# Optimization experiments

Hardware: AMD Instinct MI355X
Metric: run time of the kernel (lower is better)

The kernel has to match this reference:

```python
import jax, jax.numpy as jnp
import numpy as np

N_NODES = 20000
N_RELS = 64
RP = 8
EMB = 64
N_CLASSES = 16
NT = 250000      # unique (subject, object) pairs
N_TRIPLES = 500000


def setup_inputs() -> dict:
    rng = np.random.default_rng(0)
    # sample candidate (s, o) pairs, dedupe (mirrors torch.unique(pairs, dim=0)),
    # keep exactly NT unique pairs
    cand = rng.integers(0, N_NODES, size=(NT + 60000, 2))
    pairs = np.unique(cand, axis=0)
    assert pairs.shape[0] >= NT
    pairs = pairs[:NT]
    # each triple maps to a unique-pair row and a relation column;
    # relation_matrix is the coalesced sparse_coo (nt, num_rels) densified
    row = rng.integers(0, NT, size=N_TRIPLES)
    rel = rng.integers(0, N_RELS, size=N_TRIPLES)
    relation_matrix = np.zeros((NT, N_RELS), dtype=np.float32)
    np.add.at(relation_matrix, (row, rel), 1.0)
    # hindices / vindices exactly as in __init__ (note the literal o*r / s*r):
    s, o = pairs[:, 0].astype(np.int64), pairs[:, 1].astype(np.int64)
    rm = np.arange(RP, dtype=np.int64)[:, None]
    hrow = np.tile(s, RP)                      # (RP*NT,) row in [0, N)
    hcol = (o[None, :] * rm).reshape(-1)       # (RP*NT,) col in [0, N*RP)
    vrow = (s[None, :] * rm).reshape(-1)       # (RP*NT,) row in [0, N*RP)
    vcol = np.tile(o, RP)                      # (RP*NT,) col in [0, N)

    key = jax.random.key(0)
    ks = jax.random.split(key, 6)

    def xavier(k, shape, fan_in, fan_out):
        gain = np.float32(np.sqrt(2.0))  # calculate_gain('relu')
        bound = gain * np.float32(np.sqrt(6.0 / (fan_in + fan_out)))
        return jax.random.uniform(k, shape, jnp.float32, -bound, bound)

    lb = np.float32(1.0 / np.sqrt(N_RELS))  # nn.Linear default init bound
    return {
        "relation_matrix": jnp.asarray(relation_matrix),
        "hrow": jnp.asarray(hrow), "hcol": jnp.asarray(hcol),
        "vrow": jnp.asarray(vrow), "vcol": jnp.asarray(vcol),
        "W_l1": jax.random.uniform(ks[0], (N_RELS, RP), jnp.float32, -lb, lb),
        "b_l1": jax.random.uniform(ks[1], (RP,), jnp.float32, -lb, lb),
        "W_l2": jax.random.uniform(ks[2], (N_RELS, RP), jnp.float32, -lb, lb),
        "b_l2": jax.random.uniform(ks[3], (RP,), jnp.float32, -lb, lb),
        "weights1": xavier(ks[4], (RP, N_NODES, EMB), N_NODES * EMB, RP * EMB),
        "weights2": xavier(ks[5], (RP, EMB, N_CLASSES), EMB * N_CLASSES, RP * N_CLASSES),
        "bias1": jnp.zeros((EMB,), jnp.float32),
        "bias2": jnp.zeros((N_CLASSES,), jnp.float32),
    }


def reference(relation_matrix, hrow, hcol, vrow, vcol,
              W_l1, b_l1, W_l2, b_l2, weights1, weights2, bias1, bias2):
    n, rp, e = N_NODES, RP, EMB
    nrp = n * rp
    # ---- hop 1: latent coefficients (to_latent1, ldepth=0 => single Linear)
    l1 = relation_matrix @ W_l1 + b_l1              # (NT, RP)
    l1 = l1.T.reshape(-1)                           # (RP*NT,) r-major, matches h/v index order
    # sum_sparse(hindices, l1, (n, n*rp), row=False): per-edge column-sum normalization
    colsum = jax.ops.segment_sum(l1, hcol, num_segments=nrp)
    l1 = l1 / colsum[hcol]
    # spmm over hindices: out[hrow] += l1 * weights1.view(n*rp, e)[hcol]
    Wflat = weights1.reshape(nrp, e)                # (N*RP, EMB)
    h = jax.ops.segment_sum(l1[:, None] * Wflat[hcol], hrow, num_segments=n)
    h = jax.nn.relu(h + bias1)                      # (N, EMB)
    # ---- hop 2
    l2 = jax.nn.softmax(relation_matrix @ W_l2 + b_l2, axis=1)  # (NT, RP)
    l2 = jax.nn.relu(l2.T.reshape(-1))              # (RP*NT,)
    # sum_sparse(vindices, l2, (n*rp, n), row=True): per-edge row-sum normalization
    rowsum = jax.ops.segment_sum(l2, vrow, num_segments=nrp)
    l2 = l2 / jnp.maximum(rowsum[vrow], 1e-6)
    # spmm over vindices: out[vrow] += l2 * h[vcol]
    h2 = jax.ops.segment_sum(l2[:, None] * h[vcol], vrow, num_segments=nrp)
    h2 = h2.reshape(rp, n, e)                       # (RP, N, EMB)
    logits = jnp.einsum('rhc,rnh->nc', weights2, h2) + bias2  # (N, C)
    return logits
```

## Files before the change

### kernel.cpp

```cpp
#include <hip/hip_runtime.h>
#include <hip/hip_fp16.h>

#define NT      250000
#define NN      20000
#define RP      8
#define EMB     64
#define NCLS    16
#define NRELS   64
#define REDB    64
#define KMAX    140000
#define GEMVB   977
#define RPB     79
#define HIB     977
#define MISCB   1250

__global__ __launch_bounds__(256) void k_gemv(
    const float* __restrict__ rm,
    const float* __restrict__ W1, const float* __restrict__ b1,
    const float* __restrict__ W2, const float* __restrict__ b2,
    float* __restrict__ l1, float* __restrict__ l2,
    const int* __restrict__ hrow, int* __restrict__ rowptr,
    const int* __restrict__ vcol, int* __restrict__ cnt)
{
    __shared__ float tile[256 * 20];
    int bid = blockIdx.x;
    if (bid >= GEMVB) {
        int b = bid - GEMVB;
        if (b < RPB) {
            int i = b * 256 + threadIdx.x;
            if (i > NN) return;
            int lo = 0, hi = NT;
            while (lo < hi) { int mid = (lo + hi) >> 1; if (hrow[mid] < i) lo = mid + 1; else hi = mid; }
            rowptr[i] = lo;
        } else {
            int p = (b - RPB) * 256 + threadIdx.x;
            if (p < NT) atomicAdd(&cnt[vcol[p]], 1);
        }
        return;
    }
    int t = threadIdx.x;
    int base = bid * 256;
    float a1[8], a2[8];
#pragma unroll
    for (int r = 0; r < 8; ++r) { a1[r] = b1[r]; a2[r] = b2[r]; }

#pragma unroll 1
    for (int kc = 0; kc < 4; ++kc) {
        __syncthreads();
#pragma unroll
        for (int q = 0; q < 4; ++q) {
            int i = q * 256 + t;
            int pl = i >> 2, j4 = i & 3;
            int p = base + pl;
            float4 v = make_float4(0.f, 0.f, 0.f, 0.f);
            if (p < NT) v = reinterpret_cast<const float4*>(rm)[(size_t)p * 16 + kc * 4 + j4];
            *reinterpret_cast<float4*>(&tile[pl * 20 + j4 * 4]) = v;
        }
        __syncthreads();
        float xr[16];
#pragma unroll
        for (int j4 = 0; j4 < 4; ++j4) {
            float4 v = *reinterpret_cast<const float4*>(&tile[t * 20 + j4 * 4]);
            xr[j4 * 4 + 0] = v.x; xr[j4 * 4 + 1] = v.y;
            xr[j4 * 4 + 2] = v.z; xr[j4 * 4 + 3] = v.w;
        }
#pragma unroll
        for (int kk = 0; kk < 16; ++kk) {
            float x = xr[kk];
            int k = kc * 16 + kk;
#pragma unroll
            for (int r = 0; r < 8; ++r) {
                a1[r] = fmaf(x, W1[k * 8 + r], a1[r]);
                a2[r] = fmaf(x, W2[k * 8 + r], a2[r]);
            }
        }
    }
    int p = base + t;
    if (p >= NT) return;
    float mx = a2[0];
#pragma unroll
    for (int r = 1; r < 8; ++r) mx = fmaxf(mx, a2[r]);
    float sm = 0.f;
#pragma unroll
    for (int r = 0; r < 8; ++r) { a2[r] = __expf(a2[r] - mx); sm += a2[r]; }
    float inv = 1.0f / sm;
#pragma unroll
    for (int r = 0; r < 8; ++r) a2[r] *= inv;
    float4* o1 = reinterpret_cast<float4*>(l1 + (size_t)p * 8);
    float4* o2 = reinterpret_cast<float4*>(l2 + (size_t)p * 8);
    o1[0] = make_float4(a1[0], a1[1], a1[2], a1[3]);
    o1[1] = make_float4(a1[4], a1[5], a1[6], a1[7]);
    o2[0] = make_float4(a2[0], a2[1], a2[2], a2[3]);
    o2[1] = make_float4(a2[4], a2[5], a2[6], a2[7]);
}

__global__ __launch_bounds__(1024) void k_scan(
    const int* __restrict__ cnt, int* __restrict__ cstart, int* __restrict__ cnt2)
{
    __shared__ int part[1024];
    int t = threadIdx.x;
    int base = t * 20;
    int local[20];
    int s = 0;
#pragma unroll
    for (int i = 0; i < 20; ++i) {
        int idx = base + i;
        int c = (idx < NN) ? cnt[idx] : 0;
        local[i] = s;
        s += c;
    }
    part[t] = s;
    __syncthreads();
    for (int off = 1; off < 1024; off <<= 1) {
        int v = (t >= off) ? part[t - off] : 0;
        __syncthreads();
        part[t] += v;
        __syncthreads();
    }
    int ebase = t ? part[t - 1] : 0;
#pragma unroll
    for (int i = 0; i < 20; ++i) {
        int idx = base + i;
        if (idx < NN) { cstart[idx] = ebase + local[i]; cnt2[idx] = ebase + local[i]; }
    }
    if (t == 1023) cstart[NN] = part[1023];
}

__global__ __launch_bounds__(256) void k_pos(
    const int* __restrict__ vcol, int* __restrict__ cnt2, int* __restrict__ cscidx)
{
    int p = blockIdx.x * blockDim.x + threadIdx.x;
    if (p >= NT) return;
    int o = vcol[p];
    int slot = atomicAdd(&cnt2[o], 1);
    cscidx[slot] = p;
}

__global__ __launch_bounds__(256) void k_colsum(
    const float* __restrict__ l1, const int* __restrict__ cstart,
    const int* __restrict__ cscidx, float* __restrict__ colsum)
{
    int bid = blockIdx.x;
    if (bid < NN / 4) {
        int o = bid * 4 + (threadIdx.x >> 6);
        int lane = threadIdx.x & 63;
        int qb = cstart[o], qe = cstart[o + 1];
        if (qb == qe) return;
        int j = lane >> 3, r = lane & 7;
        float sum = 0.f;
        for (int q0 = qb; q0 < qe; q0 += 8) {
            int q = q0 + j;
            if (q < qe) sum += l1[(size_t)cscidx[q] * 8 + r];
        }
        sum += __shfl_xor(sum, 8, 64);
        sum += __shfl_xor(sum, 16, 64);
        sum += __shfl_xor(sum, 32, 64);
        if (lane >= 1 && lane < 8) atomicAdd(&colsum[o * lane], sum);
    } else {
        int b2 = bid - NN / 4;
        float s = 0.f;
        for (int i = b2 * 256 + threadIdx.x; i < NT; i += REDB * 256) s += l1[(size_t)i * 8];
        __shared__ float red[256];
        red[threadIdx.x] = s;
        __syncthreads();
        for (int off = 128; off > 0; off >>= 1) {
            if (threadIdx.x < off) red[threadIdx.x] += red[threadIdx.x + off];
            __syncthreads();
        }
        if (threadIdx.x == 0) atomicAdd(&colsum[0], red[0]);
    }
}

__global__ __launch_bounds__(256) void k_contrib(
    const float* __restrict__ l1, const float* __restrict__ colsum,
    const int* __restrict__ cstart, const int* __restrict__ cscidx,
    const float* __restrict__ w1, __half* __restrict__ contrib)
{
    int o = (int)((blockIdx.x * blockDim.x + threadIdx.x) >> 6);
    int lane = threadIdx.x & 63;
    if (o >= NN) return;
    int qb = cstart[o], qe = cstart[o + 1];
    if (qb == qe) return;
    float y[8];
    y[0] = w1[lane] / colsum[0];
#pragma unroll
    for (int r = 1; r < 8; ++r) {
        int seg = o * r;
        y[r] = w1[(size_t)seg * EMB + lane] / colsum[seg];
    }
    int q = qb;
    for (; q + 1 < qe; q += 2) {
        int p0 = cscidx[q], p1 = cscidx[q + 1];
        const float4* a4 = reinterpret_cast<const float4*>(l1 + (size_t)p0 * 8);
        const float4* b4 = reinterpret_cast<const float4*>(l1 + (size_t)p1 * 8);
        float4 A = a4[0], B = a4[1], C = b4[0], D = b4[1];
        float v0 = A.x * y[0];
        v0 = fmaf(A.y, y[1], v0); v0 = fmaf(A.z, y[2], v0); v0 = fmaf(A.w, y[3], v0);
        v0 = fmaf(B.x, y[4], v0); v0 = fmaf(B.y, y[5], v0);
        v0 = fmaf(B.z, y[6], v0); v0 = fmaf(B.w, y[7], v0);
        float v1 = C.x * y[0];
        v1 = fmaf(C.y, y[1], v1); v1 = fmaf(C.z, y[2], v1); v1 = fmaf(C.w, y[3], v1);
        v1 = fmaf(D.x, y[4], v1); v1 = fmaf(D.y, y[5], v1);
        v1 = fmaf(D.z, y[6], v1); v1 = fmaf(D.w, y[7], v1);
        contrib[(size_t)p0 * EMB + lane] = __float2half(v0);
        contrib[(size_t)p1 * EMB + lane] = __float2half(v1);
    }
    if (q < qe) {
        int p0 = cscidx[q];
        const float4* a4 = reinterpret_cast<const float4*>(l1 + (size_t)p0 * 8);
        float4 A = a4[0], B = a4[1];
        float v0 = A.x * y[0];
        v0 = fmaf(A.y, y[1], v0); v0 = fmaf(A.z, y[2], v0); v0 = fmaf(A.w, y[3], v0);
        v0 = fmaf(B.x, y[4], v0); v0 = fmaf(B.y, y[5], v0);
        v0 = fmaf(B.z, y[6], v0); v0 = fmaf(B.w, y[7], v0);
        contrib[(size_t)p0 * EMB + lane] = __float2half(v0);
    }
}

__global__ __launch_bounds__(256) void k_h(
    const __half* __restrict__ contrib, const float* __restrict__ l2,
    const int* __restrict__ rowptr, const float* __restrict__ bias1,
    __half* __restrict__ h, float* __restrict__ rowsum, float* __restrict__ rs0part)
{
    int s = (int)((blockIdx.x * blockDim.x + threadIdx.x) >> 6);
    int lane = threadIdx.x & 63;
    if (s >= NN) return;
    int pb = rowptr[s], pe = rowptr[s + 1];
    float acc = 0.f;
    for (int p = pb; p < pe; ++p)
        acc += __half2float(contrib[(size_t)p * EMB + lane]);
    h[(size_t)s * EMB + lane] = __float2half(fmaxf(acc + bias1[lane], 0.f));

    float psum = 0.f;
    for (int p0 = pb + (lane >> 3); p0 < pe; p0 += 8)
        psum += l2[(size_t)p0 * 8 + (lane & 7)];
    psum += __shfl_xor(psum, 8, 64);
    psum += __shfl_xor(psum, 16, 64);
    psum += __shfl_xor(psum, 32, 64);
    if (s == 0) {
        float tt = psum;
        tt += __shfl_xor(tt, 1, 64);
        tt += __shfl_xor(tt, 2, 64);
        tt += __shfl_xor(tt, 4, 64);
        if (lane == 0) rs0part[0] = tt;
    } else {
        if (lane == 0) rs0part[s] = psum;
        else if (lane < 8) atomicAdd(&rowsum[s * lane], psum);
    }
}

__global__ __launch_bounds__(256) void k_misc(
    float* __restrict__ rs, float* __restrict__ out, const float* __restrict__ b2,
    const float* __restrict__ rs0part)
{
    int bid = blockIdx.x;
    if (bid < MISCB) {
        int i = bid * 256 + threadIdx.x;
        if (i >= 1 && i < KMAX) rs[i] = 1.0f / fmaxf(rs[i], 1e-6f);
        if (i < NN * NCLS) out[i] = b2[i & (NCLS - 1)];
    } else {
        __shared__ float red[256];
        float sv = 0.f;
        for (int i = threadIdx.x; i < NN; i += 256) sv += rs0part[i];
        red[threadIdx.x] = sv;
        __syncthreads();
        for (int off = 128; off > 0; off >>= 1) {
            if (threadIdx.x < off) red[threadIdx.x] += red[threadIdx.x + off];
            __syncthreads();
        }
        if (threadIdx.x == 0) rs[0] = 1.0f / fmaxf(red[0], 1e-6f);
    }
}

__global__ __launch_bounds__(256) void k_l2out(
    const float* __restrict__ l2, const int* __restrict__ rowptr,
    const int* __restrict__ vcol, const __half* __restrict__ h,
    const float* __restrict__ irs, const float* __restrict__ w2,
    float* __restrict__ out, float* __restrict__ Abuf0)
{
    int s = (int)((blockIdx.x * blockDim.x + threadIdx.x) >> 6);
    int lane = threadIdx.x & 63;
    if (s >= NN) return;
    int pb = rowptr[s], pe = rowptr[s + 1];
    float sc[8];
#pragma unroll
    for (int rr = 1; rr < 8; ++rr) sc[rr] = (s > 0) ? irs[s * rr] : 0.f;
    float acc[8];
#pragma unroll
    for (int r = 0; r < 8; ++r) acc[r] = 0.f;
    int p = pb;
    for (; p + 3 < pe; p += 4) {
        int o0 = vcol[p], o1 = vcol[p + 1], o2 = vcol[p + 2], o3 = vcol[p + 3];
        float hv0 = __half2float(h[(size_t)o0 * EMB + lane]);
        float hv1 = __half2float(h[(size_t)o1 * EMB + lane]);
        float hv2 = __half2float(h[(size_t)o2 * EMB + lane]);
        float hv3 = __half2float(h[(size_t)o3 * EMB + lane]);
        const float4* q4 = reinterpret_cast<const float4*>(l2 + (size_t)p * 8);
        float4 A = q4[0], B = q4[1], C = q4[2], D = q4[3];
        float4 E = q4[4], F = q4[5], G = q4[6], H = q4[7];
        acc[0] = fmaf(A.x, hv0, fmaf(C.x, hv1, fmaf(E.x, hv2, fmaf(G.x, hv3, acc[0]))));
        acc[1] = fmaf(A.y, hv0, fmaf(C.y, hv1, fmaf(E.y, hv2, fmaf(G.y, hv3, acc[1]))));
        acc[2] = fmaf(A.z, hv0, fmaf(C.z, hv1, fmaf(E.z, hv2, fmaf(G.z, hv3, acc[2]))));
        acc[3] = fmaf(A.w, hv0, fmaf(C.w, hv1, fmaf(E.w, hv2, fmaf(G.w, hv3, acc[3]))));
        acc[4] = fmaf(B.x, hv0, fmaf(D.x, hv1, fmaf(F.x, hv2, fmaf(H.x, hv3, acc[4]))));
        acc[5] = fmaf(B.y, hv0, fmaf(D.y, hv1, fmaf(F.y, hv2, fmaf(H.y, hv3, acc[5]))));
        acc[6] = fmaf(B.z, hv0, fmaf(D.z, hv1, fmaf(F.z, hv2, fmaf(H.z, hv3, acc[6]))));
        acc[7] = fmaf(B.w, hv0, fmaf(D.w, hv1, fmaf(F.w, hv2, fmaf(H.w, hv3, acc[7]))));
    }
    for (; p < pe; ++p) {
        int o0 = vcol[p];
        float hv0 = __half2float(h[(size_t)o0 * EMB + lane]);
        const float4* q4 = reinterpret_cast<const float4*>(l2 + (size_t)p * 8);
        float4 A = q4[0], B = q4[1];
        acc[0] = fmaf(A.x, hv0, acc[0]); acc[1] = fmaf(A.y, hv0, acc[1]);
        acc[2] = fmaf(A.z, hv0, acc[2]); acc[3] = fmaf(A.w, hv0, acc[3]);
        acc[4] = fmaf(B.x, hv0, acc[4]); acc[5] = fmaf(B.y, hv0, acc[5]);
        acc[6] = fmaf(B.z, hv0, acc[6]); acc[7] = fmaf(B.w, hv0, acc[7]);
    }
    if (s == 0) {
        float a = acc[0] + acc[1] + acc[2] + acc[3] +
                  acc[4] + acc[5] + acc[6] + acc[7];
        Abuf0[lane] = a;
        return;
    }
    Abuf0[(size_t)s * EMB + lane] = acc[0];
    if (pb == pe) return;
    int hq = lane >> 4, c = lane & 15;
#pragma unroll
    for (int rr = 1; rr < 8; ++rr) {
        int k = s * rr;
        int rp = k / NN;
        int n  = k - rp * NN;
        float v = 0.f;
#pragma unroll
        for (int hh = 0; hh < 16; ++hh) {
            float av = __shfl(acc[rr], hq * 16 + hh, 64);
            v = fmaf(av, w2[((rp * EMB) + (hq * 16 + hh)) * NCLS + c], v);
        }
        v += __shfl_xor(v, 16, 64);
        v += __shfl_xor(v, 32, 64);
        if (lane < 16) atomicAdd(&out[(size_t)n * NCLS + lane], v * sc[rr]);
    }
}

__global__ __launch_bounds__(256) void k_redA(
    const float* __restrict__ Abuf0, const float* __restrict__ irs,
    const float* __restrict__ w2, float* __restrict__ out)
{
    __shared__ float red[256];
    __shared__ float part[64];
    int lane = threadIdx.x & 63, w = threadIdx.x >> 6;
    float sum = 0.f;
    for (int ss = blockIdx.x + 64 * w; ss < NN; ss += 256)
        sum += Abuf0[(size_t)ss * EMB + lane];
    red[threadIdx.x] = sum;
    __syncthreads();
    if (threadIdx.x < 64) {
        part[threadIdx.x] = red[threadIdx.x] + red[threadIdx.x + 64] +
                            red[threadIdx.x + 128] + red[threadIdx.x + 192];
    }
    __syncthreads();
    if (threadIdx.x < 64) {
        int hq = threadIdx.x >> 4, c = threadIdx.x & 15;
        float v = 0.f;
#pragma unroll
        for (int hh = 0; hh < 16; ++hh) {
            int hd = hq * 16 + hh;
            v = fmaf(part[hd], w2[hd * NCLS + c], v);
        }
        v += __shfl_xor(v, 16, 64);
        v += __shfl_xor(v, 32, 64);
        if (threadIdx.x < 16) atomicAdd(&out[c], v * irs[0]);
    }
}

extern "C" void kernel_launch(void* const* d_in, const int* in_sizes, int n_in,
                              void* d_out, int out_size, void* d_ws, size_t ws_size,
                              hipStream_t stream)
{
    const float* rm    = (const float*)d_in[0];
    const int*   hrow  = (const int*)d_in[1];
    const int*   vcol  = (const int*)d_in[4];
    const float* W1    = (const float*)d_in[5];
    const float* b1    = (const float*)d_in[6];
    const float* W2    = (const float*)d_in[7];
    const float* b2    = (const float*)d_in[8];
    const float* w1    = (const float*)d_in[9];
    const float* w2    = (const float*)d_in[10];
    const float* bias1 = (const float*)d_in[11];
    const float* bias2 = (const float*)d_in[12];
    float* out = (float*)d_out;

    float* ws = (float*)d_ws;
    float*  l1      = ws;
    float*  l2      = ws + 2000000;
    int*    rowptr  = (int*)(ws + 4000000);
    float*  colsum  = ws + 4100000;
    float*  rowsum  = ws + 4260000;
    __half* h       = (__half*)(ws + 4400000);
    int*    cnt     = (int*)(ws + 5040000);
    int*    cstart  = cnt + 20000;
    int*    cnt2    = cstart + 20001;
    int*    cscidx  = cnt2 + 20000;
    __half* contrib = (__half*)(ws + 5600000);
    float*  Abuf0   = ws;
    float*  rs0part = ws + 1280000;

    hipMemsetAsync(colsum, 0, (size_t)160000 * sizeof(float), stream);
    hipMemsetAsync(rowsum, 0, (size_t)KMAX * sizeof(float), stream);
    hipMemsetAsync(cnt, 0, (size_t)20000 * sizeof(int), stream);

    k_gemv   <<<GEMVB + RPB + HIB, 256, 0, stream>>>(rm, W1, b1, W2, b2, l1, l2,
                                                     hrow, rowptr, vcol, cnt);
    k_scan   <<<1, 1024, 0, stream>>>(cnt, cstart, cnt2);
    k_pos    <<<(NT + 255) / 256, 256, 0, stream>>>(vcol, cnt2, cscidx);
    k_colsum <<<NN / 4 + REDB, 256, 0, stream>>>(l1, cstart, cscidx, colsum);
    k_contrib<<<(NN * 64) / 256, 256, 0, stream>>>(l1, colsum, cstart, cscidx, w1, contrib);
    k_h      <<<(NN * 64) / 256, 256, 0, stream>>>(contrib, l2, rowptr, bias1, h, rowsum, rs0part);
    k_misc   <<<MISCB + 1, 256, 0, stream>>>(rowsum, out, bias2, rs0part);
    k_l2out  <<<(NN * 64) / 256, 256, 0, stream>>>(l2, rowptr, vcol, h, rowsum, w2, out, Abuf0);
    k_redA   <<<64, 256, 0, stream>>>(Abuf0, rowsum, w2, out);
}
```

Before: 233.5 us.

## Remove k_misc by folding its work into neighbouring kernels

New measurement: 233.2 us. Within noise of the previous version (-0.1%).

```diff
diff --git a/kernel.cpp b/kernel.cpp
--- a/kernel.cpp
+++ b/kernel.cpp
@@ -12,7 +12,7 @@
 #define GEMVB   977
 #define RPB     79
 #define HIB     977
-#define MISCB   1250
+#define OIB     1250
 
 __global__ __launch_bounds__(256) void k_gemv(
     const float* __restrict__ rm,
@@ -20,7 +20,8 @@
     const float* __restrict__ W2, const float* __restrict__ b2,
     float* __restrict__ l1, float* __restrict__ l2,
     const int* __restrict__ hrow, int* __restrict__ rowptr,
-    const int* __restrict__ vcol, int* __restrict__ cnt)
+    const int* __restrict__ vcol, int* __restrict__ cnt,
+    float* __restrict__ out, const float* __restrict__ bias2)
 {
     __shared__ float tile[256 * 20];
     int bid = blockIdx.x;
@@ -32,9 +33,12 @@
             int lo = 0, hi = NT;
             while (lo < hi) { int mid = (lo + hi) >> 1; if (hrow[mid] < i) lo = mid + 1; else hi = mid; }
             rowptr[i] = lo;
-        } else {
+        } else if (b < RPB + HIB) {
             int p = (b - RPB) * 256 + threadIdx.x;
             if (p < NT) atomicAdd(&cnt[vcol[p]], 1);
+        } else {
+            int i = (b - RPB - HIB) * 256 + threadIdx.x;
+            if (i < NN * NCLS) out[i] = bias2[i & (NCLS - 1)];
         }
         return;
     }
@@ -189,11 +193,14 @@
         y[r] = w1[(size_t)seg * EMB + lane] / colsum[seg];
     }
     int q = qb;
-    for (; q + 1 < qe; q += 2) {
-        int p0 = cscidx[q], p1 = cscidx[q + 1];
+    for (; q + 3 < qe; q += 4) {
+        int p0 = cscidx[q], p1 = cscidx[q + 1], p2 = cscidx[q + 2], p3 = cscidx[q + 3];
         const float4* a4 = reinterpret_cast<const float4*>(l1 + (size_t)p0 * 8);
         const float4* b4 = reinterpret_cast<const float4*>(l1 + (size_t)p1 * 8);
+        const float4* c4 = reinterpret_cast<const float4*>(l1 + (size_t)p2 * 8);
+        const float4* d4 = reinterpret_cast<const float4*>(l1 + (size_t)p3 * 8);
         float4 A = a4[0], B = a4[1], C = b4[0], D = b4[1];
+        float4 E = c4[0], F = c4[1], G = d4[0], H = d4[1];
         float v0 = A.x * y[0];
         v0 = fmaf(A.y, y[1], v0); v0 = fmaf(A.z, y[2], v0); v0 = fmaf(A.w, y[3], v0);
         v0 = fmaf(B.x, y[4], v0); v0 = fmaf(B.y, y[5], v0);
@@ -202,10 +209,20 @@
         v1 = fmaf(C.y, y[1], v1); v1 = fmaf(C.z, y[2], v1); v1 = fmaf(C.w, y[3], v1);
         v1 = fmaf(D.x, y[4], v1); v1 = fmaf(D.y, y[5], v1);
         v1 = fmaf(D.z, y[6], v1); v1 = fmaf(D.w, y[7], v1);
+        float v2 = E.x * y[0];
+        v2 = fmaf(E.y, y[1], v2); v2 = fmaf(E.z, y[2], v2); v2 = fmaf(E.w, y[3], v2);
+        v2 = fmaf(F.x, y[4], v2); v2 = fmaf(F.y, y[5], v2);
+        v2 = fmaf(F.z, y[6], v2); v2 = fmaf(F.w, y[7], v2);
+        float v3 = G.x * y[0];
+        v3 = fmaf(G.y, y[1], v3); v3 = fmaf(G.z, y[2], v3); v3 = fmaf(G.w, y[3], v3);
+        v3 = fmaf(H.x, y[4], v3); v3 = fmaf(H.y, y[5], v3);
+        v3 = fmaf(H.z, y[6], v3); v3 = fmaf(H.w, y[7], v3);
         contrib[(size_t)p0 * EMB + lane] = __float2half(v0);
         contrib[(size_t)p1 * EMB + lane] = __float2half(v1);
-    }
-    if (q < qe) {
+        contrib[(size_t)p2 * EMB + lane] = __float2half(v2);
+        contrib[(size_t)p3 * EMB + lane] = __float2half(v3);
+    }
+    for (; q < qe; ++q) {
         int p0 = cscidx[q];
         const float4* a4 = reinterpret_cast<const float4*>(l1 + (size_t)p0 * 8);
         float4 A = a4[0], B = a4[1];
@@ -249,33 +266,10 @@
     }
 }
 
-__global__ __launch_bounds__(256) void k_misc(
-    float* __restrict__ rs, float* __restrict__ out, const float* __restrict__ b2,
-    const float* __restrict__ rs0part)
-{
-    int bid = blockIdx.x;
-    if (bid < MISCB) {
-        int i = bid * 256 + threadIdx.x;
-        if (i >= 1 && i < KMAX) rs[i] = 1.0f / fmaxf(rs[i], 1e-6f);
-        if (i < NN * NCLS) out[i] = b2[i & (NCLS - 1)];
-    } else {
-        __shared__ float red[256];
-        float sv = 0.f;
-        for (int i = threadIdx.x; i < NN; i += 256) sv += rs0part[i];
-        red[threadIdx.x] = sv;
-        __syncthreads();
-        for (int off = 128; off > 0; off >>= 1) {
-            if (threadIdx.x < off) red[threadIdx.x] += red[threadIdx.x + off];
-            __syncthreads();
-        }
-        if (threadIdx.x == 0) rs[0] = 1.0f / fmaxf(red[0], 1e-6f);
-    }
-}
-
 __global__ __launch_bounds__(256) void k_l2out(
     const float* __restrict__ l2, const int* __restrict__ rowptr,
     const int* __restrict__ vcol, const __half* __restrict__ h,
-    const float* __restrict__ irs, const float* __restrict__ w2,
+    const float* __restrict__ rowsum, const float* __restrict__ w2,
     float* __restrict__ out, float* __restrict__ Abuf0)
 {
     int s = (int)((blockIdx.x * blockDim.x + threadIdx.x) >> 6);
@@ -284,7 +278,8 @@
     int pb = rowptr[s], pe = rowptr[s + 1];
     float sc[8];
 #pragma unroll
-    for (int rr = 1; rr < 8; ++rr) sc[rr] = (s > 0) ? irs[s * rr] : 0.f;
+    for (int rr = 1; rr < 8; ++rr)
+        sc[rr] = (s > 0) ? (1.0f / fmaxf(rowsum[s * rr], 1e-6f)) : 0.f;
     float acc[8];
 #pragma unroll
     for (int r = 0; r < 8; ++r) acc[r] = 0.f;
@@ -344,11 +339,23 @@
 }
 
 __global__ __launch_bounds__(256) void k_redA(
-    const float* __restrict__ Abuf0, const float* __restrict__ irs,
+    const float* __restrict__ Abuf0, const float* __restrict__ rs0part,
     const float* __restrict__ w2, float* __restrict__ out)
 {
     __shared__ float red[256];
     __shared__ float part[64];
+    __shared__ float irs0s;
+    float sv = 0.f;
+    for (int i = threadIdx.x; i < NN; i += 256) sv += rs0part[i];
+    red[threadIdx.x] = sv;
+    __syncthreads();
+    for (int off = 128; off > 0; off >>= 1) {
+        if (threadIdx.x < off) red[threadIdx.x] += red[threadIdx.x + off];
+        __syncthreads();
+    }
+    if (threadIdx.x == 0) irs0s = 1.0f / fmaxf(red[0], 1e-6f);
+    __syncthreads();
+    float irs0 = irs0s;
     int lane = threadIdx.x & 63, w = threadIdx.x >> 6;
     float sum = 0.f;
     for (int ss = blockIdx.x + 64 * w; ss < NN; ss += 256)
@@ -370,7 +377,7 @@
         }
         v += __shfl_xor(v, 16, 64);
         v += __shfl_xor(v, 32, 64);
-        if (threadIdx.x < 16) atomicAdd(&out[c], v * irs[0]);
+        if (threadIdx.x < 16) atomicAdd(&out[c], v * irs0);
     }
 }
 
@@ -406,18 +413,16 @@
     float*  Abuf0   = ws;
     float*  rs0part = ws + 1280000;
 
-    hipMemsetAsync(colsum, 0, (size_t)160000 * sizeof(float), stream);
-    hipMemsetAsync(rowsum, 0, (size_t)KMAX * sizeof(float), stream);
+    hipMemsetAsync(colsum, 0, (size_t)300000 * sizeof(float), stream);
     hipMemsetAsync(cnt, 0, (size_t)20000 * sizeof(int), stream);
 
-    k_gemv   <<<GEMVB + RPB + HIB, 256, 0, stream>>>(rm, W1, b1, W2, b2, l1, l2,
-                                                     hrow, rowptr, vcol, cnt);
+    k_gemv   <<<GEMVB + RPB + HIB + OIB, 256, 0, stream>>>(rm, W1, b1, W2, b2, l1, l2,
+                                                           hrow, rowptr, vcol, cnt, out, bias2);
     k_scan   <<<1, 1024, 0, stream>>>(cnt, cstart, cnt2);
     k_pos    <<<(NT + 255) / 256, 256, 0, stream>>>(vcol, cnt2, cscidx);
     k_colsum <<<NN / 4 + REDB, 256, 0, stream>>>(l1, cstart, cscidx, colsum);
     k_contrib<<<(NN * 64) / 256, 256, 0, stream>>>(l1, colsum, cstart, cscidx, w1, contrib);
     k_h      <<<(NN * 64) / 256, 256, 0, stream>>>(contrib, l2, rowptr, bias1, h, rowsum, rs0part);
-    k_misc   <<<MISCB + 1, 256, 0, stream>>>(rowsum, out, bias2, rs0part);
     k_l2out  <<<(NN * 64) / 256, 256, 0, stream>>>(l2, rowptr, vcol, h, rowsum, w2, out, Abuf0);
-    k_redA   <<<64, 256, 0, stream>>>(Abuf0, rowsum, w2, out);
-}
+    k_redA   <<<64, 256, 0, stream>>>(Abuf0, rs0part, w2, out);
+}
```
